# Kernel optimization log

Measured on AMD Instinct MI355X. Metric: run time of the kernel, lower is better.

Reference implementation:

```python
import jax, jax.numpy as jnp
import numpy as np

B = 4096       # batch
D = 256        # num_features
H = 512        # proposal_hidden_units
K = 10         # mixture_components
C = 64         # context_units
L = 4          # proposal_residual_blocks
S = 10         # num_importance_samples (call default)
HEAD = 3 * K + C
LOG2PI = float(np.log(2.0 * np.pi))


def setup_inputs() -> dict:
    key = jax.random.key(0)
    ks = jax.random.split(key, 10)
    x = jax.random.normal(ks[0], (B, D), jnp.float32)
    observed_mask = (jax.random.uniform(ks[1], (B, D)) < 0.5).astype(jnp.float32)
    s_in = 1.0 / np.sqrt(2 * D)
    s_h = 1.0 / np.sqrt(H)
    W_in = (jax.random.normal(ks[2], (2 * D, H), jnp.float32) * s_in)
    b_in = jnp.zeros((H,), jnp.float32)
    W1 = jax.random.normal(ks[3], (L, H, H), jnp.float32) * s_h
    b1 = jnp.zeros((L, H), jnp.float32)
    W2 = jax.random.normal(ks[4], (L, H, H), jnp.float32) * s_h
    b2 = jnp.zeros((L, H), jnp.float32)
    W_fin = jax.random.normal(ks[5], (H, D * HEAD), jnp.float32) * s_h
    b_fin = jnp.zeros((D * HEAD,), jnp.float32)
    return {
        "x": x, "observed_mask": observed_mask,
        "W_in": W_in, "b_in": b_in,
        "W1": W1, "b1": b1, "W2": W2, "b2": b2,
        "W_fin": W_fin, "b_fin": b_fin,
        "num_importance_samples": S,
    }


def _proposal_params(x_o, observed_mask, W_in, b_in, W1, b1, W2, b2, W_fin, b_fin):
    # Residual MLP proposal network on [x_o, observed_mask].
    h = jnp.concatenate([x_o, observed_mask], axis=-1) @ W_in + b_in  # [B, H]
    for l in range(L):
        r = jax.nn.relu(h) @ W1[l] + b1[l]
        r = jax.nn.relu(r) @ W2[l] + b2[l]
        h = h + r
    out = (h @ W_fin + b_fin).reshape(h.shape[0], D, HEAD)  # [B, D, 3K+C]
    logits = out[..., :K]
    means = out[..., K:2 * K]
    scales = jax.nn.softplus(out[..., 2 * K:3 * K]) + 1e-3
    return logits, means, scales


def reference(x, observed_mask, W_in, b_in, W1, b1, W2, b2, W_fin, b_fin,
              num_importance_samples):
    query = 1.0 - observed_mask
    x_o = x * observed_mask
    x_u = x * query

    logits, means, scales = _proposal_params(
        x_o, observed_mask, W_in, b_in, W1, b1, W2, b2, W_fin, b_fin)

    # Per-feature mixture-of-Gaussians log-likelihood of x_u, masked by query.
    log_w = jax.nn.log_softmax(logits, axis=-1)               # [B, D, K]
    z = (x_u[..., None] - means) / scales
    comp_ll = -0.5 * z * z - jnp.log(scales) - 0.5 * LOG2PI   # [B, D, K]
    proposal_ll = jax.scipy.special.logsumexp(log_w + comp_ll, axis=-1) * query

    # Samples (stop_gradient in the original).
    skey = jax.random.key(1234)
    kc, kn = jax.random.split(skey)
    comp = jax.random.categorical(kc, logits, axis=-1,
                                  shape=(num_importance_samples,) + logits.shape[:2])  # [S, B, D]
    mu = jnp.take_along_axis(means[None], comp[..., None], axis=-1)[..., 0]    # [S, B, D]
    sg = jnp.take_along_axis(scales[None], comp[..., None], axis=-1)[..., 0]   # [S, B, D]
    eps = jax.random.normal(kn, comp.shape, jnp.float32)
    samples = mu + sg * eps                                   # [S, B, D]
    samples = jnp.transpose(samples, (1, 0, 2))               # [B, S, D]
    samples = jax.lax.stop_gradient(samples) * query[:, None, :]
    # call() multiplies by query twice (before and after selected_features block)
    proposal_samples = samples * query[:, None, :]

    proposal_mean = jnp.sum(jax.nn.softmax(logits, axis=-1) * means, axis=-1) * query
    proposal_mean = proposal_mean * query  # second masking, as in call()

    return proposal_ll, proposal_samples, proposal_mean
```

## Files before the change

### kernel.cpp

```cpp
#include <hip/hip_runtime.h>
#include <cstdint>

#define B 4096
#define D 256
#define H 512
#define K 10
#define NL 4
#define S 10
#define NOUT 30
#define HEADW 94
#define ND (B*D)
#define NFIN 7680

__host__ __device__ inline void threefry2x32(uint32_t k0, uint32_t k1,
                                             uint32_t x0, uint32_t x1,
                                             uint32_t& o0, uint32_t& o1) {
  uint32_t ks2 = k0 ^ k1 ^ 0x1BD11BDAu;
#define TF_ROT(x, r) (((x) << (r)) | ((x) >> (32 - (r))))
#define TF_RND(r) { x0 += x1; x1 = TF_ROT(x1, r); x1 ^= x0; }
  x0 += k0; x1 += k1;
  TF_RND(13) TF_RND(15) TF_RND(26) TF_RND(6)
  x0 += k1; x1 += ks2 + 1u;
  TF_RND(17) TF_RND(29) TF_RND(16) TF_RND(24)
  x0 += ks2; x1 += k0 + 2u;
  TF_RND(13) TF_RND(15) TF_RND(26) TF_RND(6)
  x0 += k0; x1 += k1 + 3u;
  TF_RND(17) TF_RND(29) TF_RND(16) TF_RND(24)
  x0 += k1; x1 += ks2 + 4u;
  TF_RND(13) TF_RND(15) TF_RND(26) TF_RND(6)
  x0 += ks2; x1 += k0 + 5u;
  o0 = x0; o1 = x1;
#undef TF_RND
#undef TF_ROT
}

__device__ __forceinline__ uint32_t rb32(uint32_t k0, uint32_t k1, uint32_t idx) {
  uint32_t a, b;
  threefry2x32(k0, k1, 0u, idx, a, b);
  return a ^ b;
}

__device__ __forceinline__ float u01_from_bits(uint32_t bits) {
  return __uint_as_float((bits >> 9) | 0x3f800000u) - 1.0f;
}

__device__ __forceinline__ float erfinv_f32(float x) {
  float w = -log1pf(-x * x);
  float p;
  if (w < 5.0f) {
    w = w - 2.5f;
    p = 2.81022636e-08f;
    p = fmaf(p, w, 3.43273939e-07f);
    p = fmaf(p, w, -3.5233877e-06f);
    p = fmaf(p, w, -4.39150654e-06f);
    p = fmaf(p, w, 0.00021858087f);
    p = fmaf(p, w, -0.00125372503f);
    p = fmaf(p, w, -0.00417768164f);
    p = fmaf(p, w, 0.246640727f);
    p = fmaf(p, w, 1.50140941f);
  } else {
    w = sqrtf(w) - 3.0f;
    p = -0.000200214257f;
    p = fmaf(p, w, 0.000100950558f);
    p = fmaf(p, w, 0.00134934322f);
    p = fmaf(p, w, -0.00367342844f);
    p = fmaf(p, w, 0.00573950773f);
    p = fmaf(p, w, -0.0076224613f);
    p = fmaf(p, w, 0.00943887047f);
    p = fmaf(p, w, 1.00167406f);
    p = fmaf(p, w, 2.83297682f);
  }
  return p * x;
}

__device__ __forceinline__ void gload16(const void* g, void* l) {
  __builtin_amdgcn_global_load_lds(
      (const __attribute__((address_space(1))) void*)g,
      (__attribute__((address_space(3))) void*)l, 16, 0, 0);
}

__global__ __launch_bounds__(256) void prep_kernel(const float* __restrict__ x,
                                                   const float* __restrict__ mask,
                                                   float* __restrict__ xcat) {
  int i = blockIdx.x * 256 + threadIdx.x;
  if (i >= B * 2 * D) return;
  int b = i >> 9, c = i & 511;
  float v = (c < D) ? x[b * D + c] * mask[b * D + c] : mask[b * D + (c - D)];
  xcat[i] = v;
}

__global__ __launch_bounds__(256) void wgather(const float* __restrict__ Wf,
                                               float* __restrict__ wsg) {
  int c = blockIdx.x * 256 + threadIdx.x;
  int k = blockIdx.y;
  int dd = c / NOUT, j = c - dd * NOUT;
  wsg[(size_t)k * NFIN + c] = Wf[(size_t)k * (D * HEADW) + dd * HEADW + j];
}

template <int RELU, int RES>
__global__ __launch_bounds__(256) void gemm_trunk(const float* __restrict__ A,
                                                  const float* __restrict__ W,
                                                  const float* __restrict__ bias,
                                                  const float* res, float* C) {
  __shared__ float As[32 * 68];
  __shared__ float Ws[32 * 64];
  const int tid = threadIdx.x;
  const int lane = tid & 63, wid = tid >> 6;
  const int tx = tid & 15, ty = tid >> 4;
  const int bm = blockIdx.y * 64, bn = blockIdx.x * 64;
  const int ls = tid & 7, lm = tid >> 3;

  float acc[4][4] = {};

  for (int k0 = 0; k0 < H; k0 += 32) {
#pragma unroll
    for (int c = wid; c < 8; c += 4) {
      gload16(W + (size_t)(k0 + c * 4 + (lane >> 4)) * H + bn + (lane & 15) * 4,
              Ws + c * 256 + lane * 4);
    }
#pragma unroll
    for (int r = 0; r < 2; ++r) {
      int m = lm + 32 * r;
      float4 f = *(const float4*)(A + (size_t)(bm + m) * H + k0 + 4 * ls);
      if (RELU) {
        f.x = fmaxf(f.x, 0.0f); f.y = fmaxf(f.y, 0.0f);
        f.z = fmaxf(f.z, 0.0f); f.w = fmaxf(f.w, 0.0f);
      }
      As[(4 * ls + 0) * 68 + m] = f.x;
      As[(4 * ls + 1) * 68 + m] = f.y;
      As[(4 * ls + 2) * 68 + m] = f.z;
      As[(4 * ls + 3) * 68 + m] = f.w;
    }
    __syncthreads();
#pragma unroll
    for (int kk = 0; kk < 32; ++kk) {
      float4 a4 = *(const float4*)(As + kk * 68 + ty * 4);
      float4 b4 = *(const float4*)(Ws + kk * 64 + tx * 4);
      float a[4] = {a4.x, a4.y, a4.z, a4.w};
      float b[4] = {b4.x, b4.y, b4.z, b4.w};
#pragma unroll
      for (int i = 0; i < 4; ++i)
#pragma unroll
        for (int j = 0; j < 4; ++j) acc[i][j] = fmaf(a[i], b[j], acc[i][j]);
    }
    __syncthreads();
  }
#pragma unroll
  for (int i = 0; i < 4; ++i) {
    int row = bm + ty * 4 + i;
#pragma unroll
    for (int j = 0; j < 4; ++j) {
      int col = bn + tx * 4 + j;
      float v = acc[i][j] + bias[col];
      if (RES) v = res[(size_t)row * H + col] + v;
      C[(size_t)row * H + col] = v;
    }
  }
}

__global__ __launch_bounds__(256) void gemm_fin(const float* __restrict__ A,
                                                const float* __restrict__ Wg,
                                                const float* __restrict__ bf,
                                                float* __restrict__ headout) {
  __shared__ float As[32 * 136];
  __shared__ float Ws[32 * 128];
  const int tid = threadIdx.x;
  const int lane = tid & 63, wid = tid >> 6;
  const int tx = tid & 15, ty = tid >> 4;
  const int bm = blockIdx.y * 128, bn = blockIdx.x * 128;
  const int ls = tid & 7, lm = tid >> 3;

  float acc[8][8] = {};

  for (int k0 = 0; k0 < H; k0 += 32) {
#pragma unroll
    for (int c = wid; c < 16; c += 4) {
      gload16(Wg + (size_t)(k0 + c * 2 + (lane >> 5)) * NFIN + bn + (lane & 31) * 4,
              Ws + c * 256 + lane * 4);
    }
#pragma unroll
    for (int r = 0; r < 4; ++r) {
      int m = lm + 32 * r;
      float4 f = *(const float4*)(A + (size_t)(bm + m) * H + k0 + 4 * ls);
      As[(4 * ls + 0) * 136 + m] = f.x;
      As[(4 * ls + 1) * 136 + m] = f.y;
      As[(4 * ls + 2) * 136 + m] = f.z;
      As[(4 * ls + 3) * 136 + m] = f.w;
    }
    __syncthreads();
#pragma unroll
    for (int kk = 0; kk < 32; ++kk) {
      float a[8], b[8];
      *(float4*)(a + 0) = *(const float4*)(As + kk * 136 + ty * 8);
      *(float4*)(a + 4) = *(const float4*)(As + kk * 136 + ty * 8 + 4);
      *(float4*)(b + 0) = *(const float4*)(Ws + kk * 128 + tx * 8);
      *(float4*)(b + 4) = *(const float4*)(Ws + kk * 128 + tx * 8 + 4);
#pragma unroll
      for (int i = 0; i < 8; ++i)
#pragma unroll
        for (int j = 0; j < 8; ++j) acc[i][j] = fmaf(a[i], b[j], acc[i][j]);
    }
    __syncthreads();
  }
#pragma unroll
  for (int i = 0; i < 8; ++i) {
    int row = bm + ty * 8 + i;
#pragma unroll
    for (int j = 0; j < 8; ++j) {
      int c = bn + tx * 8 + j;
      int dd = c / NOUT, jj = c - dd * NOUT;
      float v = acc[i][j] + bf[dd * HEADW + jj];
      if (jj >= 2 * K) {
        v = (fmaxf(v, 0.0f) + log1pf(expf(-fabsf(v)))) + 0.001f;
      }
      headout[(size_t)row * NFIN + c] = v;
    }
  }
}

__global__ __launch_bounds__(256) void ll_mean_kernel(const float* __restrict__ head,
                                                      const float* __restrict__ x,
                                                      const float* __restrict__ mask,
                                                      float* __restrict__ out_ll,
                                                      float* __restrict__ out_mean) {
  int idx = blockIdx.x * 256 + threadIdx.x;
  if (idx >= ND) return;
  const float* hp = head + (size_t)idx * NOUT;
  float lg[K], mn[K], sc[K];
#pragma unroll
  for (int k = 0; k < K; ++k) { lg[k] = hp[k]; mn[k] = hp[K + k]; sc[k] = hp[2 * K + k]; }
  float q = 1.0f - mask[idx];
  float xu = x[idx] * q;
  float m = lg[0];
#pragma unroll
  for (int k = 1; k < K; ++k) m = fmaxf(m, lg[k]);
  float e[K];
  float sum = 0.0f;
#pragma unroll
  for (int k = 0; k < K; ++k) { e[k] = expf(lg[k] - m); sum += e[k]; }
  float lse = logf(sum);
  float a[K];
  float amax = -3.402823466e38f;
#pragma unroll
  for (int k = 0; k < K; ++k) {
    float z = (xu - mn[k]) / sc[k];
    float cll = -0.5f * z * z - logf(sc[k]) - 0.9189385332046727f;
    float lw = (lg[k] - m) - lse;
    a[k] = lw + cll;
    amax = fmaxf(amax, a[k]);
  }
  float s2 = 0.0f;
#pragma unroll
  for (int k = 0; k < K; ++k) s2 += expf(a[k] - amax);
  out_ll[idx] = (logf(s2) + amax) * q;
  float pm = 0.0f;
#pragma unroll
  for (int k = 0; k < K; ++k) pm += (e[k] / sum) * mn[k];
  out_mean[idx] = pm * q;
}

__global__ __launch_bounds__(256) void sample_kernel(const float* __restrict__ head,
                                                     const float* __restrict__ mask,
                                                     float* __restrict__ out_s,
                                                     uint32_t kc0, uint32_t kc1,
                                                     uint32_t kn0, uint32_t kn1) {
  int tid = blockIdx.x * 256 + threadIdx.x;
  if (tid >= ND * S) return;
  int s = tid >> 20;
  int idx = tid & (ND - 1);
  int b = idx >> 8, d = idx & (D - 1);
  float q = 1.0f - mask[idx];
  const float* hp = head + (size_t)idx * NOUT;
  uint32_t base = (uint32_t)tid * (uint32_t)K;
  int best = 0;
  float vbest = -3.402823466e38f;
#pragma unroll
  for (int k = 0; k < K; ++k) {
    uint32_t bits = rb32(kc0, kc1, base + (uint32_t)k);
    float f = fmaxf(u01_from_bits(bits), 1.17549435e-38f);
    float g = -logf(-logf(f));
    float v = g + hp[k];
    if (v > vbest) { vbest = v; best = k; }
  }
  uint32_t ebits = rb32(kn0, kn1, (uint32_t)tid);
  float f = u01_from_bits(ebits);
  float r = f * 2.0f + (-0.99999994f);
  r = fmaxf(r, -0.99999994f);
  float eps = 1.4142135623730951f * erfinv_f32(r);
  float mu = hp[K + best];
  float sg = hp[2 * K + best];
  out_s[((size_t)b * S + s) * D + d] = (mu + sg * eps) * q;
}

extern "C" void kernel_launch(void* const* d_in, const int* in_sizes, int n_in,
                              void* d_out, int out_size, void* d_ws, size_t ws_size,
                              hipStream_t stream) {
  const float* x    = (const float*)d_in[0];
  const float* mask = (const float*)d_in[1];
  const float* W_in = (const float*)d_in[2];
  const float* b_in = (const float*)d_in[3];
  const float* W1   = (const float*)d_in[4];
  const float* b1   = (const float*)d_in[5];
  const float* W2   = (const float*)d_in[6];
  const float* b2   = (const float*)d_in[7];
  const float* Wf   = (const float*)d_in[8];
  const float* bf   = (const float*)d_in[9];

  char* w = (char*)d_ws;
  float* head = (float*)w;
  float* xcat = head;
  float* t    = head;
  float* h    = (float*)(w + 125829120);
  float* wsg  = (float*)(w + 134217728);

  float* out_ll   = (float*)d_out;
  float* out_s    = out_ll + (size_t)ND;
  float* out_mean = out_s + (size_t)ND * S;

  wgather<<<dim3(NFIN / 256, 512), 256, 0, stream>>>(Wf, wsg);

  prep_kernel<<<(B * 2 * D) / 256, 256, 0, stream>>>(x, mask, xcat);

  dim3 gtr(H / 64, B / 64);
  gemm_trunk<0, 0><<<gtr, 256, 0, stream>>>(xcat, W_in, b_in, nullptr, h);
  for (int l = 0; l < NL; ++l) {
    gemm_trunk<1, 0><<<gtr, 256, 0, stream>>>(h, W1 + (size_t)l * H * H,
                                              b1 + (size_t)l * H, nullptr, t);
    gemm_trunk<1, 1><<<gtr, 256, 0, stream>>>(t, W2 + (size_t)l * H * H,
                                              b2 + (size_t)l * H, h, h);
  }

  gemm_fin<<<dim3(NFIN / 128, B / 128), 256, 0, stream>>>(h, wsg, bf, head);

  ll_mean_kernel<<<ND / 256, 256, 0, stream>>>(head, x, mask, out_ll, out_mean);

  uint32_t kc0, kc1, kn0, kn1;
  threefry2x32(0u, 1234u, 0u, 0u, kc0, kc1);
  threefry2x32(0u, 1234u, 0u, 1u, kn0, kn1);
  sample_kernel<<<(ND * S) / 256, 256, 0, stream>>>(head, mask, out_s, kc0, kc1, kn0, kn1);
}
```

Baseline: 1.332 ms.

## Split head GEMM into fp32 logits and split-bf16 MFMA means/scales, fuse tail kernels

The final head GEMM is split in two. Logits stay in fp32 SIMT so the argmax in sampling is unchanged. Means and scales go through a 3-product hi/lo bf16 MFMA GEMM that approximates fp32 accuracy. The ll/mean and sampling kernels are fused into one kernel that reads the head once per element and loops over the samples. The trunk GEMM tile is also doubled in M. The trade is extra weight-splitting preprocessing and small precision differences in means and scales.

```diff
diff --git a/kernel.cpp b/kernel.cpp
--- a/kernel.cpp
+++ b/kernel.cpp
@@ -11,6 +11,11 @@
 #define HEADW 94
 #define ND (B*D)
 #define NFIN 7680
+#define NLOG 2560
+#define NMS  5120
+
+typedef __bf16 bf16x8 __attribute__((ext_vector_type(8)));
+typedef float  f32x16 __attribute__((ext_vector_type(16)));
 
 __host__ __device__ inline void threefry2x32(uint32_t k0, uint32_t k1,
                                              uint32_t x0, uint32_t x1,
@@ -73,10 +78,33 @@
   return p * x;
 }
 
+__device__ __forceinline__ unsigned short bf16_rne(float x) {
+  uint32_t u = __float_as_uint(x);
+  uint32_t r = u + 0x7fffu + ((u >> 16) & 1u);
+  return (unsigned short)(r >> 16);
+}
+
+__device__ __forceinline__ void split2(float x, short& hi, short& lo) {
+  unsigned short hb = bf16_rne(x);
+  float hf = __uint_as_float((uint32_t)hb << 16);
+  hi = (short)hb;
+  lo = (short)bf16_rne(x - hf);
+}
+
 __device__ __forceinline__ void gload16(const void* g, void* l) {
   __builtin_amdgcn_global_load_lds(
       (const __attribute__((address_space(1))) void*)g,
       (__attribute__((address_space(3))) void*)l, 16, 0, 0);
+}
+
+template <int ROWS>
+__device__ __forceinline__ void stage_region(const short* __restrict__ g,
+                                             short* l, int wid, int lane) {
+#pragma unroll
+  for (int c = wid; c < ROWS / 16; c += 4) {
+    const short* gp = g + (size_t)(c * 16 + (lane >> 2)) * 512 + (lane & 3) * 8;
+    gload16(gp, l + c * 512);
+  }
 }
 
 __global__ __launch_bounds__(256) void prep_kernel(const float* __restrict__ x,
@@ -89,12 +117,38 @@
   xcat[i] = v;
 }
 
-__global__ __launch_bounds__(256) void wgather(const float* __restrict__ Wf,
-                                               float* __restrict__ wsg) {
+__global__ __launch_bounds__(256) void wgatherL(const float* __restrict__ Wf,
+                                                float* __restrict__ wsgL) {
   int c = blockIdx.x * 256 + threadIdx.x;
   int k = blockIdx.y;
-  int dd = c / NOUT, j = c - dd * NOUT;
-  wsg[(size_t)k * NFIN + c] = Wf[(size_t)k * (D * HEADW) + dd * HEADW + j];
+  int dd = c / K, j = c - dd * K;
+  wsgL[(size_t)k * NLOG + c] = Wf[(size_t)k * (D * HEADW) + dd * HEADW + j];
+}
+
+__global__ __launch_bounds__(256) void wsplit_ms(const float* __restrict__ Wf,
+                                                 short* __restrict__ whi,
+                                                 short* __restrict__ wlo) {
+  __shared__ float tile[32][33];
+  int n0 = blockIdx.x * 32, k0 = blockIdx.y * 32;
+  int tx = threadIdx.x & 31, ty = threadIdx.x >> 5;
+#pragma unroll
+  for (int r = 0; r < 4; ++r) {
+    int k = k0 + ty + r * 8;
+    int n = n0 + tx;
+    int dd = n / 20, j = n - dd * 20;
+    tile[ty + r * 8][tx] = Wf[(size_t)k * (D * HEADW) + dd * HEADW + 10 + j];
+  }
+  __syncthreads();
+#pragma unroll
+  for (int r = 0; r < 4; ++r) {
+    int n = n0 + ty + r * 8;
+    int k = k0 + tx;
+    float v = tile[tx][ty + r * 8];
+    short hb, lb;
+    split2(v, hb, lb);
+    whi[(size_t)n * 512 + k] = hb;
+    wlo[(size_t)n * 512 + k] = lb;
+  }
 }
 
 template <int RELU, int RES>
@@ -102,15 +156,15 @@
                                                   const float* __restrict__ W,
                                                   const float* __restrict__ bias,
                                                   const float* res, float* C) {
-  __shared__ float As[32 * 68];
+  __shared__ float As[32 * 136];
   __shared__ float Ws[32 * 64];
   const int tid = threadIdx.x;
   const int lane = tid & 63, wid = tid >> 6;
   const int tx = tid & 15, ty = tid >> 4;
-  const int bm = blockIdx.y * 64, bn = blockIdx.x * 64;
+  const int bm = blockIdx.y * 128, bn = blockIdx.x * 64;
   const int ls = tid & 7, lm = tid >> 3;
 
-  float acc[4][4] = {};
+  float acc[8][4] = {};
 
   for (int k0 = 0; k0 < H; k0 += 32) {
 #pragma unroll
@@ -119,35 +173,35 @@
               Ws + c * 256 + lane * 4);
     }
 #pragma unroll
-    for (int r = 0; r < 2; ++r) {
+    for (int r = 0; r < 4; ++r) {
       int m = lm + 32 * r;
       float4 f = *(const float4*)(A + (size_t)(bm + m) * H + k0 + 4 * ls);
       if (RELU) {
         f.x = fmaxf(f.x, 0.0f); f.y = fmaxf(f.y, 0.0f);
         f.z = fmaxf(f.z, 0.0f); f.w = fmaxf(f.w, 0.0f);
       }
-      As[(4 * ls + 0) * 68 + m] = f.x;
-      As[(4 * ls + 1) * 68 + m] = f.y;
-      As[(4 * ls + 2) * 68 + m] = f.z;
-      As[(4 * ls + 3) * 68 + m] = f.w;
+      As[(4 * ls + 0) * 136 + m] = f.x;
+      As[(4 * ls + 1) * 136 + m] = f.y;
+      As[(4 * ls + 2) * 136 + m] = f.z;
+      As[(4 * ls + 3) * 136 + m] = f.w;
     }
     __syncthreads();
 #pragma unroll
     for (int kk = 0; kk < 32; ++kk) {
-      float4 a4 = *(const float4*)(As + kk * 68 + ty * 4);
-      float4 b4 = *(const float4*)(Ws + kk * 64 + tx * 4);
-      float a[4] = {a4.x, a4.y, a4.z, a4.w};
-      float b[4] = {b4.x, b4.y, b4.z, b4.w};
-#pragma unroll
-      for (int i = 0; i < 4; ++i)
+      float a[8], b[4];
+      *(float4*)(a + 0) = *(const float4*)(As + kk * 136 + ty * 8);
+      *(float4*)(a + 4) = *(const float4*)(As + kk * 136 + ty * 8 + 4);
+      *(float4*)(b + 0) = *(const float4*)(Ws + kk * 64 + tx * 4);
+#pragma unroll
+      for (int i = 0; i < 8; ++i)
 #pragma unroll
         for (int j = 0; j < 4; ++j) acc[i][j] = fmaf(a[i], b[j], acc[i][j]);
     }
     __syncthreads();
   }
 #pragma unroll
-  for (int i = 0; i < 4; ++i) {
-    int row = bm + ty * 4 + i;
+  for (int i = 0; i < 8; ++i) {
+    int row = bm + ty * 8 + i;
 #pragma unroll
     for (int j = 0; j < 4; ++j) {
       int col = bn + tx * 4 + j;
@@ -158,10 +212,10 @@
   }
 }
 
-__global__ __launch_bounds__(256) void gemm_fin(const float* __restrict__ A,
-                                                const float* __restrict__ Wg,
-                                                const float* __restrict__ bf,
-                                                float* __restrict__ headout) {
+__global__ __launch_bounds__(256) void gemm_logits(const float* __restrict__ A,
+                                                   const float* __restrict__ Wg,
+                                                   const float* __restrict__ bf,
+                                                   float* __restrict__ headout) {
   __shared__ float As[32 * 136];
   __shared__ float Ws[32 * 128];
   const int tid = threadIdx.x;
@@ -175,7 +229,7 @@
   for (int k0 = 0; k0 < H; k0 += 32) {
 #pragma unroll
     for (int c = wid; c < 16; c += 4) {
-      gload16(Wg + (size_t)(k0 + c * 2 + (lane >> 5)) * NFIN + bn + (lane & 31) * 4,
+      gload16(Wg + (size_t)(k0 + c * 2 + (lane >> 5)) * NLOG + bn + (lane & 31) * 4,
               Ws + c * 256 + lane * 4);
     }
 #pragma unroll
@@ -208,23 +262,112 @@
 #pragma unroll
     for (int j = 0; j < 8; ++j) {
       int c = bn + tx * 8 + j;
-      int dd = c / NOUT, jj = c - dd * NOUT;
+      int dd = c / K, jj = c - dd * K;
       float v = acc[i][j] + bf[dd * HEADW + jj];
-      if (jj >= 2 * K) {
-        v = (fmaxf(v, 0.0f) + log1pf(expf(-fabsf(v)))) + 0.001f;
+      headout[(size_t)row * NFIN + dd * NOUT + jj] = v;
+    }
+  }
+}
+
+__global__ __launch_bounds__(256) void gemm_ms(const float* __restrict__ A,
+                                               const short* __restrict__ Bh,
+                                               const short* __restrict__ Bl,
+                                               const float* __restrict__ bf,
+                                               float* __restrict__ headout) {
+  __shared__ short lds[4 * 128 * 32];
+  const int tid = threadIdx.x;
+  const int lane = tid & 63, wid = tid >> 6;
+  const int wm = wid >> 1, wn = wid & 1;
+  const int bm = blockIdx.y * 128, bn = blockIdx.x * 128;
+  const int ls = tid & 7, lm = tid >> 3;
+
+  short* ldsAh = lds;
+  short* ldsAl = lds + 4096;
+  short* ldsBh = lds + 8192;
+  short* ldsBl = lds + 12288;
+
+  const short* gBh = Bh + (size_t)bn * 512;
+  const short* gBl = Bl + (size_t)bn * 512;
+
+  f32x16 acc[2][2];
+#pragma unroll
+  for (int mt = 0; mt < 2; ++mt)
+#pragma unroll
+    for (int nt = 0; nt < 2; ++nt)
+#pragma unroll
+      for (int i = 0; i < 16; ++i) acc[mt][nt][i] = 0.0f;
+
+  for (int k0 = 0; k0 < 512; k0 += 32) {
+    stage_region<128>(gBh + k0, ldsBh, wid, lane);
+    stage_region<128>(gBl + k0, ldsBl, wid, lane);
+#pragma unroll
+    for (int r = 0; r < 4; ++r) {
+      int m = lm + 32 * r;
+      float4 f = *(const float4*)(A + (size_t)(bm + m) * H + k0 + 4 * ls);
+      short4 h4, l4;
+      split2(f.x, h4.x, l4.x); split2(f.y, h4.y, l4.y);
+      split2(f.z, h4.z, l4.z); split2(f.w, h4.w, l4.w);
+      *(short4*)(ldsAh + m * 32 + 4 * ls) = h4;
+      *(short4*)(ldsAl + m * 32 + 4 * ls) = l4;
+    }
+    __syncthreads();
+#pragma unroll
+    for (int sub = 0; sub < 2; ++sub) {
+      bf16x8 ah[2], al[2], bh[2], bl[2];
+#pragma unroll
+      for (int mt = 0; mt < 2; ++mt) {
+        int r = wm * 64 + mt * 32 + (lane & 31);
+        int off = r * 32 + sub * 16 + (lane >> 5) * 8;
+        ah[mt] = *(const bf16x8*)(ldsAh + off);
+        al[mt] = *(const bf16x8*)(ldsAl + off);
       }
-      headout[(size_t)row * NFIN + c] = v;
-    }
-  }
-}
-
-__global__ __launch_bounds__(256) void ll_mean_kernel(const float* __restrict__ head,
-                                                      const float* __restrict__ x,
-                                                      const float* __restrict__ mask,
-                                                      float* __restrict__ out_ll,
-                                                      float* __restrict__ out_mean) {
+#pragma unroll
+      for (int nt = 0; nt < 2; ++nt) {
+        int r = wn * 64 + nt * 32 + (lane & 31);
+        int off = r * 32 + sub * 16 + (lane >> 5) * 8;
+        bh[nt] = *(const bf16x8*)(ldsBh + off);
+        bl[nt] = *(const bf16x8*)(ldsBl + off);
+      }
+#pragma unroll
+      for (int mt = 0; mt < 2; ++mt)
+#pragma unroll
+        for (int nt = 0; nt < 2; ++nt) {
+          acc[mt][nt] = __builtin_amdgcn_mfma_f32_32x32x16_bf16(ah[mt], bh[nt], acc[mt][nt], 0, 0, 0);
+          acc[mt][nt] = __builtin_amdgcn_mfma_f32_32x32x16_bf16(ah[mt], bl[nt], acc[mt][nt], 0, 0, 0);
+          acc[mt][nt] = __builtin_amdgcn_mfma_f32_32x32x16_bf16(al[mt], bh[nt], acc[mt][nt], 0, 0, 0);
+        }
+    }
+    __syncthreads();
+  }
+
+#pragma unroll
+  for (int mt = 0; mt < 2; ++mt)
+#pragma unroll
+    for (int nt = 0; nt < 2; ++nt) {
+      int col = bn + wn * 64 + nt * 32 + (lane & 31);
+      int rbase = bm + wm * 64 + mt * 32 + 4 * (lane >> 5);
+      int dd = col / 20, j = col - dd * 20;
+#pragma unroll
+      for (int reg = 0; reg < 16; ++reg) {
+        int row = rbase + (reg & 3) + 8 * (reg >> 2);
+        float v = acc[mt][nt][reg] + bf[dd * HEADW + 10 + j];
+        if (j >= 10) v = (fmaxf(v, 0.0f) + log1pf(expf(-fabsf(v)))) + 0.001f;
+        headout[(size_t)row * NFIN + dd * NOUT + 10 + j] = v;
+      }
+    }
+}
+
+__global__ __launch_bounds__(256) void fused_tail(const float* __restrict__ head,
+                                                  const float* __restrict__ x,
+                                                  const float* __restrict__ mask,
+                                                  float* __restrict__ out_ll,
+                                                  float* __restrict__ out_s,
+                                                  float* __restrict__ out_mean,
+                                                  uint32_t kc0, uint32_t kc1,
+                                                  uint32_t kn0, uint32_t kn1) {
   int idx = blockIdx.x * 256 + threadIdx.x;
   if (idx >= ND) return;
+  int b = idx >> 8, d = idx & (D - 1);
   const float* hp = head + (size_t)idx * NOUT;
   float lg[K], mn[K], sc[K];
 #pragma unroll
@@ -257,39 +400,26 @@
 #pragma unroll
   for (int k = 0; k < K; ++k) pm += (e[k] / sum) * mn[k];
   out_mean[idx] = pm * q;
-}
-
-__global__ __launch_bounds__(256) void sample_kernel(const float* __restrict__ head,
-                                                     const float* __restrict__ mask,
-                                                     float* __restrict__ out_s,
-                                                     uint32_t kc0, uint32_t kc1,
-                                                     uint32_t kn0, uint32_t kn1) {
-  int tid = blockIdx.x * 256 + threadIdx.x;
-  if (tid >= ND * S) return;
-  int s = tid >> 20;
-  int idx = tid & (ND - 1);
-  int b = idx >> 8, d = idx & (D - 1);
-  float q = 1.0f - mask[idx];
-  const float* hp = head + (size_t)idx * NOUT;
-  uint32_t base = (uint32_t)tid * (uint32_t)K;
-  int best = 0;
-  float vbest = -3.402823466e38f;
-#pragma unroll
-  for (int k = 0; k < K; ++k) {
-    uint32_t bits = rb32(kc0, kc1, base + (uint32_t)k);
-    float f = fmaxf(u01_from_bits(bits), 1.17549435e-38f);
-    float g = -logf(-logf(f));
-    float v = g + hp[k];
-    if (v > vbest) { vbest = v; best = k; }
-  }
-  uint32_t ebits = rb32(kn0, kn1, (uint32_t)tid);
-  float f = u01_from_bits(ebits);
-  float r = f * 2.0f + (-0.99999994f);
-  r = fmaxf(r, -0.99999994f);
-  float eps = 1.4142135623730951f * erfinv_f32(r);
-  float mu = hp[K + best];
-  float sg = hp[2 * K + best];
-  out_s[((size_t)b * S + s) * D + d] = (mu + sg * eps) * q;
+  for (int s = 0; s < S; ++s) {
+    uint32_t t32 = (uint32_t)s * (uint32_t)ND + (uint32_t)idx;
+    uint32_t base = t32 * (uint32_t)K;
+    int best = 0;
+    float vbest = -3.402823466e38f;
+#pragma unroll
+    for (int k = 0; k < K; ++k) {
+      uint32_t bits = rb32(kc0, kc1, base + (uint32_t)k);
+      float f = fmaxf(u01_from_bits(bits), 1.17549435e-38f);
+      float g = -logf(-logf(f));
+      float v = g + lg[k];
+      if (v > vbest) { vbest = v; best = k; }
+    }
+    uint32_t ebits = rb32(kn0, kn1, t32);
+    float f = u01_from_bits(ebits);
+    float r = f * 2.0f + (-0.99999994f);
+    r = fmaxf(r, -0.99999994f);
+    float eps = 1.4142135623730951f * erfinv_f32(r);
+    out_s[((size_t)b * S + s) * D + d] = (mn[best] + sc[best] * eps) * q;
+  }
 }
 
 extern "C" void kernel_launch(void* const* d_in, const int* in_sizes, int n_in,
@@ -307,21 +437,24 @@
   const float* bf   = (const float*)d_in[9];
 
   char* w = (char*)d_ws;
-  float* head = (float*)w;
-  float* xcat = head;
-  float* t    = head;
-  float* h    = (float*)(w + 125829120);
-  float* wsg  = (float*)(w + 134217728);
+  float* head  = (float*)w;
+  float* xcat  = head;
+  float* t     = head;
+  float* h     = (float*)(w + 125829120);
+  float* wsgL  = (float*)(w + 134217728);
+  short* wms_h = (short*)(w + 139460608);
+  short* wms_l = (short*)(w + 144703488);
 
   float* out_ll   = (float*)d_out;
   float* out_s    = out_ll + (size_t)ND;
   float* out_mean = out_s + (size_t)ND * S;
 
-  wgather<<<dim3(NFIN / 256, 512), 256, 0, stream>>>(Wf, wsg);
+  wgatherL<<<dim3(NLOG / 256, 512), 256, 0, stream>>>(Wf, wsgL);
+  wsplit_ms<<<dim3(NMS / 32, 512 / 32), 256, 0, stream>>>(Wf, wms_h, wms_l);
 
   prep_kernel<<<(B * 2 * D) / 256, 256, 0, stream>>>(x, mask, xcat);
 
-  dim3 gtr(H / 64, B / 64);
+  dim3 gtr(H / 64, B / 128);
   gemm_trunk<0, 0><<<gtr, 256, 0, stream>>>(xcat, W_in, b_in, nullptr, h);
   for (int l = 0; l < NL; ++l) {
     gemm_trunk<1, 0><<<gtr, 256, 0, stream>>>(h, W1 + (size_t)l * H * H,
@@ -330,12 +463,12 @@
                                               b2 + (size_t)l * H, h, h);
   }
 
-  gemm_fin<<<dim3(NFIN / 128, B / 128), 256, 0, stream>>>(h, wsg, bf, head);
-
-  ll_mean_kernel<<<ND / 256, 256, 0, stream>>>(head, x, mask, out_ll, out_mean);
+  gemm_logits<<<dim3(NLOG / 128, B / 128), 256, 0, stream>>>(h, wsgL, bf, head);
+  gemm_ms<<<dim3(NMS / 128, B / 128), 256, 0, stream>>>(h, wms_h, wms_l, bf, head);
 
   uint32_t kc0, kc1, kn0, kn1;
   threefry2x32(0u, 1234u, 0u, 0u, kc0, kc1);
   threefry2x32(0u, 1234u, 0u, 1u, kn0, kn1);
-  sample_kernel<<<(ND * S) / 256, 256, 0, stream>>>(head, mask, out_s, kc0, kc1, kn0, kn1);
-}
+  fused_tail<<<ND / 256, 256, 0, stream>>>(head, x, mask, out_ll, out_s, out_mean,
+                                           kc0, kc1, kn0, kn1);
+}
```

After: 1.322 ms. About the same (-0.8%).
